# Optimization experiments

Hardware: AMD Instinct MI355X
Metric: run time of the kernel (lower is better)

Reference implementation:

```python
import jax, jax.numpy as jnp
import numpy as np

N_NODES = 100000
N_EDGES = 1600000
D_IN = 64
D_OUT = 64
N_AGGR = 2   # mean, std
N_SCAL = 3   # identity, amplification, attenuation
EPS = 1e-7


def setup_inputs() -> dict:
    key = jax.random.key(0)
    ks = jax.random.split(key, 6)
    x = jax.random.normal(ks[0], (N_NODES, D_IN), dtype=jnp.float32)
    edge_row = jax.random.randint(ks[1], (N_EDGES,), 0, N_NODES)  # dst nodes
    edge_col = jax.random.randint(ks[2], (N_EDGES,), 0, N_NODES)  # src nodes
    # glorot init for linear weights, stored as [out, in] like torch.nn.Linear
    g = np.sqrt(6.0 / (D_IN + D_OUT))
    pre_w = jax.random.uniform(ks[3], (N_AGGR, N_SCAL, D_OUT, D_IN),
                               minval=-g, maxval=g, dtype=jnp.float32)
    lin_w = jax.random.uniform(ks[4], (D_OUT, D_IN), minval=-g, maxval=g,
                               dtype=jnp.float32)
    bias = jnp.zeros((D_OUT,), dtype=jnp.float32)
    # avg_deg['log'] = mean over nodes of log(deg+1); use expected value ~log(17)
    avg_deg_log = jnp.asarray(np.log(17.0), dtype=jnp.float32)
    return {"x": x, "edge_row": edge_row, "edge_col": edge_col,
            "pre_w": pre_w, "lin_w": lin_w, "bias": bias,
            "avg_deg_log": avg_deg_log}


def reference(x, edge_row, edge_col, pre_w, lin_w, bias, avg_deg_log):
    n = x.shape[0]
    # deg = adj_t.storage.rowcount(): number of edges per destination node
    deg = jax.ops.segment_sum(jnp.ones_like(edge_row, dtype=x.dtype),
                              edge_row, num_segments=n)[:, None]  # [N,1]
    # Two SpMM passes: adj_t @ x and adj_t @ x**2 (sum over source neighbors)
    xj = x[edge_col]                                             # [E,D]
    s1 = jax.ops.segment_sum(xj, edge_row, num_segments=n)       # [N,D]
    s2 = jax.ops.segment_sum(xj * xj, edge_row, num_segments=n)  # [N,D]
    mean = s1
    std = jnp.sqrt(jax.nn.relu(s2 - s1 * s1) + EPS)
    agg = jnp.stack([mean, std])                                 # [2,N,D]
    # 6 per-head projections: heads ordered as product(aggregators, scalers)
    proj = jnp.einsum('and,asod->asno', agg, pre_w)              # [2,3,N,O]
    logd = jnp.log(deg + 1.0)                                    # [N,1]
    factors = jnp.stack([
        jnp.ones_like(logd),            # identity
        logd / avg_deg_log,             # amplification
        avg_deg_log / (logd + EPS),     # attenuation
    ])                                                           # [3,N,1]
    out = (proj * factors[None]).sum(axis=(0, 1))                # sum over heads
    out = out + x @ lin_w.T + bias
    return out
```

## Files before the change

kernel.cpp:

```cpp
#include <hip/hip_runtime.h>
#include <cmath>

constexpr int KTOT = 448;
constexpr int KSTEPS = 14;
constexpr int ZROW = 456;
constexpr int NBMAX = 256;
constexpr int BCAP = 12288;

typedef __attribute__((ext_vector_type(8))) short bf16x8;
typedef __attribute__((ext_vector_type(4))) float f32x4;

static __device__ inline ushort bfq(float f) {
  unsigned u = __builtin_bit_cast(unsigned, f);
  return (ushort)((u + 0x7FFFu + ((u >> 16) & 1u)) >> 16);
}
static __device__ inline float b2f(ushort h) {
  return __builtin_bit_cast(float, (unsigned)h << 16);
}
static __device__ inline unsigned pk2(float a, float b) {
  return (unsigned)bfq(a) | ((unsigned)bfq(b) << 16);
}

__global__ void __launch_bounds__(256)
kA_prep(const float* __restrict__ x, ushort* __restrict__ xh,
        const float* __restrict__ pre_w, const float* __restrict__ lin_w,
        float* __restrict__ Wt, ushort* __restrict__ Bfrag,
        int* __restrict__ bcur, int total) {
  int t = threadIdx.x;
  if (blockIdx.x == 0) bcur[t] = t * BCAP;

  int base = blockIdx.x * 2048 + t * 8;
  if (base + 7 < total) {
    const float4* xp = (const float4*)(x + base);
    float4 v0 = xp[0], v1 = xp[1];
    uint4 o;
    o.x = pk2(v0.x, v0.y);
    o.y = pk2(v0.z, v0.w);
    o.z = pk2(v1.x, v1.y);
    o.w = pk2(v1.z, v1.w);
    *(uint4*)(xh + base) = o;
  }

  int idx = blockIdx.x * 256 + t;
  if (idx < KTOT * 64) {
    int k = idx >> 6, o = idx & 63;
    int slot = k >> 6, d = k & 63;
    Wt[idx] = (slot < 6) ? pre_w[slot * 4096 + o * 64 + d] : lin_w[o * 64 + d];
    int j = idx & 7, lane = (idx >> 3) & 63, ot = (idx >> 9) & 3, ks = idx >> 11;
    int kk = ks * 32 + (lane >> 4) * 8 + j;
    int oo = ot * 16 + (lane & 15);
    int s2 = kk >> 6, d2 = kk & 63;
    float v = (s2 < 6) ? pre_w[s2 * 4096 + oo * 64 + d2] : lin_w[oo * 64 + d2];
    Bfrag[idx] = bfq(v);
  }
}

#define BTILE 8192
__global__ void __launch_bounds__(256)
kD_binpass(const int* __restrict__ erow, const int* __restrict__ ecol,
           int* __restrict__ bcur, unsigned* __restrict__ pairs, int ne) {
  __shared__ int h[NBMAX], gb[NBMAX], h2[NBMAX];
  int t = threadIdx.x;
  h[t] = 0; h2[t] = 0;
  __syncthreads();
  int base = blockIdx.x * BTILE;
  int lim = ne - base; if (lim > BTILE) lim = BTILE;
  for (int k = t; k < lim; k += 256)
    atomicAdd(&h[erow[base + k] >> 9], 1);
  __syncthreads();
  if (h[t] > 0) gb[t] = atomicAdd(&bcur[t], h[t]);
  __syncthreads();
  for (int k = t; k < lim; k += 256) {
    int dst = erow[base + k];
    int src = ecol[base + k];
    int b = dst >> 9;
    int r = atomicAdd(&h2[b], 1);
    pairs[gb[b] + r] = ((unsigned)(dst & 511) << 17) | (unsigned)src;
  }
}

__global__ void __launch_bounds__(512)
kE_within(const unsigned* __restrict__ pairs, const int* __restrict__ bcur,
          int2* __restrict__ rr, int* __restrict__ esrc, int nn) {
  __shared__ int lcnt[512], ts[512];
  int b = blockIdx.x;
  int t = threadIdx.x;
  int nstart = b << 9;
  int s = b * BCAP;
  int m = bcur[b] - s;
  lcnt[t] = 0;
  __syncthreads();
  for (int i = t; i < m; i += 512)
    atomicAdd(&lcnt[pairs[s + i] >> 17], 1);
  __syncthreads();
  int v = lcnt[t];
  ts[t] = v;
  __syncthreads();
  for (int off = 1; off < 512; off <<= 1) {
    int u = (t >= off) ? ts[t - off] : 0;
    __syncthreads();
    ts[t] += u;
    __syncthreads();
  }
  int incl = ts[t];
  int n = nstart + t;
  if (n < nn) rr[n] = make_int2(s + incl - v, s + incl);
  lcnt[t] = s + incl - v;
  __syncthreads();
  for (int i = t; i < m; i += 512) {
    unsigned w = pairs[s + i];
    int p = atomicAdd(&lcnt[w >> 17], 1);
    esrc[p] = (int)(w & 0x1FFFFu);
  }
}

static __device__ inline void chunk_acc(const ushort* __restrict__ xh, int sv,
                                        int cnt, int lane, float& a1, float& a2) {
  int k = 0;
  for (; k + 15 < cnt; k += 16) {
    float v[16];
#pragma unroll
    for (int u = 0; u < 16; ++u)
      v[u] = b2f(xh[__shfl(sv, k + u) * 64 + lane]);
#pragma unroll
    for (int u = 0; u < 16; ++u) { a1 += v[u]; a2 = fmaf(v[u], v[u], a2); }
  }
  for (; k + 3 < cnt; k += 4) {
    float v[4];
#pragma unroll
    for (int u = 0; u < 4; ++u)
      v[u] = b2f(xh[__shfl(sv, k + u) * 64 + lane]);
#pragma unroll
    for (int u = 0; u < 4; ++u) { a1 += v[u]; a2 = fmaf(v[u], v[u], a2); }
  }
  for (; k < cnt; ++k) {
    float v = b2f(xh[__shfl(sv, k) * 64 + lane]);
    a1 += v; a2 = fmaf(v, v, a2);
  }
}

__global__ void __launch_bounds__(256, 6)
k_agg_dense(const ushort* __restrict__ xh,
            const int2* __restrict__ rr,
            const int* __restrict__ esrc,
            const ushort* __restrict__ Bfrag,
            const float* __restrict__ Wt,
            const float* __restrict__ bias,
            const float* __restrict__ avgp,
            float* __restrict__ out, int nn) {
  __shared__ __align__(16) ushort zs[16 * ZROW];
  const float avg = avgp[0];
  const int wave = threadIdx.x >> 6, lane = threadIdx.x & 63;
  const int n0 = blockIdx.x * 16;
  const int nw = n0 + wave * 4;

  int2 rv = (lane < 4) ? rr[nw + lane] : make_int2(0, 0);
  int s0 = __shfl(rv.x, 0), t0 = __shfl(rv.y, 0);
  int s1 = __shfl(rv.x, 1), t1 = __shfl(rv.y, 1);
  int s2 = __shfl(rv.x, 2), t2 = __shfl(rv.y, 2);
  int s3 = __shfl(rv.x, 3), t3 = __shfl(rv.y, 3);
  int sv0 = (s0 + lane < t0) ? esrc[s0 + lane] : 0;
  int sv1 = (s1 + lane < t1) ? esrc[s1 + lane] : 0;
  int sv2 = (s2 + lane < t2) ? esrc[s2 + lane] : 0;
  int sv3 = (s3 + lane < t3) ? esrc[s3 + lane] : 0;

  int zmask = 0;

#define DO_NODE(J, SJ, EJ, SVJ)                                              \
  {                                                                          \
    int n = nw + J;                                                          \
    float a1 = 0.f, a2 = 0.f;                                                \
    int nb = EJ - SJ; if (nb > 64) nb = 64;                                  \
    chunk_acc(xh, SVJ, nb, lane, a1, a2);                                    \
    for (int base = SJ + 64; base < EJ; base += 64) {                        \
      int c = EJ - base; if (c > 64) c = 64;                                 \
      int sv = (base + lane < EJ) ? esrc[base + lane] : 0;                   \
      chunk_acc(xh, sv, c, lane, a1, a2);                                    \
    }                                                                        \
    float m = a1;                                                            \
    float sd = sqrtf(fmaxf(a2 - m * m, 0.f) + 1e-7f);                        \
    int deg = EJ - SJ;                                                       \
    if (deg == 0) zmask |= (1 << J);                                         \
    float logd = logf((float)deg + 1.f);                                     \
    float f2 = logd / avg;                                                   \
    float f3 = avg / (logd + 1e-7f);                                         \
    float xv = b2f(xh[n * 64 + lane]);    \
    ushort* zr = zs + (wave * 4 + J) * ZROW;                                 \
    zr[lane]       = bfq(m);                                                 \
    zr[64 + lane]  = bfq(m * f2);                                            \
    zr[128 + lane] = bfq(m * f3);                                            \
    zr[192 + lane] = bfq(sd);                                                \
    zr[256 + lane] = bfq(sd * f2);                                           \
    zr[320 + lane] = bfq(sd * f3);                                           \
    zr[384 + lane] = bfq(xv);                                                \
  }
  DO_NODE(0, s0, t0, sv0)
  DO_NODE(1, s1, t1, sv1)
  DO_NODE(2, s2, t2, sv2)
  DO_NODE(3, s3, t3, sv3)
#undef DO_NODE

  __syncthreads();

  const int r = lane & 15, kg = lane >> 4;
  const ushort* za = zs + r * ZROW + kg * 8;
  const ushort* bp = Bfrag + (wave * 64 + lane) * 8;
  f32x4 acc = {0.f, 0.f, 0.f, 0.f};
#pragma unroll
  for (int ks = 0; ks < KSTEPS; ++ks) {
    bf16x8 a = *(const bf16x8*)(za + ks * 32);
    bf16x8 b = *(const bf16x8*)(bp + ks * 2048);
    acc = __builtin_amdgcn_mfma_f32_16x16x32_bf16(a, b, acc, 0, 0, 0);
  }
  float bc = bias[wave * 16 + r];
#pragma unroll
  for (int i = 0; i < 4; ++i) {
    int n = n0 + kg * 4 + i;
    if (n < nn) out[n * 64 + wave * 16 + r] = acc[i] + bc;
  }

  if (__syncthreads_or(zmask)) {
#pragma unroll
    for (int J = 0; J < 4; ++J) {
      int n = nw + J;
      if ((zmask >> J) & 1 && n < nn) {
        float sd0 = sqrtf(1e-7f);
        float f3z = avg / 1e-7f;
        float accx = bias[lane];
        for (int d = 0; d < 64; ++d) {
          float xd = b2f(xh[n * 64 + d]);
          accx += sd0 * Wt[(192 + d) * 64 + lane]
                + sd0 * f3z * Wt[(320 + d) * 64 + lane]
                + xd * Wt[(384 + d) * 64 + lane];
        }
        out[n * 64 + lane] = accx;
      }
    }
  }
}

extern "C" void kernel_launch(void* const* d_in, const int* in_sizes, int n_in,
                              void* d_out, int out_size, void* d_ws, size_t ws_size,
                              hipStream_t stream) {
  const float* x     = (const float*)d_in[0];
  const int*   erow  = (const int*)d_in[1];
  const int*   ecol  = (const int*)d_in[2];
  const float* pre_w = (const float*)d_in[3];
  const float* lin_w = (const float*)d_in[4];
  const float* bias  = (const float*)d_in[5];
  const float* avgp  = (const float*)d_in[6];
  float* out = (float*)d_out;

  int nn = in_sizes[0] / 64;
  int ne = in_sizes[1];
  int total = nn * 64;
  int nbk = (nn + 511) / 512;

  char* w = (char*)d_ws;
  auto align = [](size_t v) { return (v + 255) & ~(size_t)255; };
  size_t off = 0;
  ushort* xh     = (ushort*)(w + off); off = align(off + (size_t)total * 2);
  int* esrc      = (int*)(w + off); off = align(off + (size_t)NBMAX * BCAP * 4);
  unsigned* prs  = (unsigned*)(w + off); off = align(off + (size_t)NBMAX * BCAP * 4);
  int2* rr       = (int2*)(w + off); off = align(off + (size_t)nn * 8);
  int* bcur      = (int*)(w + off); off = align(off + NBMAX * 4);
  float* Wt      = (float*)(w + off); off = align(off + (size_t)KTOT * 64 * 4);
  ushort* Bfr    = (ushort*)(w + off); off = align(off + (size_t)KSTEPS * 4 * 64 * 8 * 2);
  (void)ws_size;

  int gA = (total + 2047) / 2048;
  kA_prep<<<gA, 256, 0, stream>>>(x, xh, pre_w, lin_w, Wt, Bfr, bcur, total);
  kD_binpass<<<(ne + BTILE - 1) / BTILE, 256, 0, stream>>>(erow, ecol, bcur, prs, ne);
  kE_within<<<nbk, 512, 0, stream>>>(prs, bcur, rr, esrc, nn);
  k_agg_dense<<<(nn + 15) / 16, 256, 0, stream>>>(xh, rr, esrc, Bfr, Wt, bias,
                                                  avgp, out, nn);
}
```

Before: 188.0 us.

## Raise block counts in edge binning and split per-bucket CSR build into halves

The binning pass now uses smaller edge tiles with 512 threads per block, which launches many more blocks. The per-bucket counting-sort kernel now runs two blocks per 512-node bucket, each handling 256 destination nodes and writing into its own half of the bucket's output region. The aim is to fill more of the GPU's compute units during the CSR construction stages. The cost is that each half-block scans the whole bucket's pair list, doubling those reads, and more blocks contend on the global bucket-cursor atomics.

```diff
diff --git a/kernel.cpp b/kernel.cpp
--- a/kernel.cpp
+++ b/kernel.cpp
@@ -55,22 +55,22 @@
   }
 }
 
-#define BTILE 8192
-__global__ void __launch_bounds__(256)
+#define BTILE 2048
+__global__ void __launch_bounds__(512)
 kD_binpass(const int* __restrict__ erow, const int* __restrict__ ecol,
            int* __restrict__ bcur, unsigned* __restrict__ pairs, int ne) {
   __shared__ int h[NBMAX], gb[NBMAX], h2[NBMAX];
   int t = threadIdx.x;
-  h[t] = 0; h2[t] = 0;
+  if (t < NBMAX) { h[t] = 0; h2[t] = 0; }
   __syncthreads();
   int base = blockIdx.x * BTILE;
   int lim = ne - base; if (lim > BTILE) lim = BTILE;
-  for (int k = t; k < lim; k += 256)
+  for (int k = t; k < lim; k += 512)
     atomicAdd(&h[erow[base + k] >> 9], 1);
   __syncthreads();
-  if (h[t] > 0) gb[t] = atomicAdd(&bcur[t], h[t]);
-  __syncthreads();
-  for (int k = t; k < lim; k += 256) {
+  if (t < NBMAX && h[t] > 0) gb[t] = atomicAdd(&bcur[t], h[t]);
+  __syncthreads();
+  for (int k = t; k < lim; k += 512) {
     int dst = erow[base + k];
     int src = ecol[base + k];
     int b = dst >> 9;
@@ -82,35 +82,45 @@
 __global__ void __launch_bounds__(512)
 kE_within(const unsigned* __restrict__ pairs, const int* __restrict__ bcur,
           int2* __restrict__ rr, int* __restrict__ esrc, int nn) {
-  __shared__ int lcnt[512], ts[512];
-  int b = blockIdx.x;
+  __shared__ int lcnt[256], ts[256];
+  int blk = blockIdx.x;
+  int b = blk >> 1, half = blk & 1;
   int t = threadIdx.x;
-  int nstart = b << 9;
+  int nstart = (b << 9) + half * 256;
   int s = b * BCAP;
   int m = bcur[b] - s;
-  lcnt[t] = 0;
-  __syncthreads();
-  for (int i = t; i < m; i += 512)
-    atomicAdd(&lcnt[pairs[s + i] >> 17], 1);
-  __syncthreads();
-  int v = lcnt[t];
-  ts[t] = v;
-  __syncthreads();
-  for (int off = 1; off < 512; off <<= 1) {
-    int u = (t >= off) ? ts[t - off] : 0;
+  int ebase = s + half * (BCAP / 2);
+  int lo = half << 8, hi = lo + 256;
+  if (t < 256) lcnt[t] = 0;
+  __syncthreads();
+  for (int i = t; i < m; i += 512) {
+    int dl = (int)(pairs[s + i] >> 17);
+    if (dl >= lo && dl < hi) atomicAdd(&lcnt[dl - lo], 1);
+  }
+  __syncthreads();
+  int v = 0;
+  if (t < 256) { v = lcnt[t]; ts[t] = v; }
+  __syncthreads();
+  for (int off = 1; off < 256; off <<= 1) {
+    int u = (t >= off && t < 256) ? ts[t - off] : 0;
     __syncthreads();
-    ts[t] += u;
+    if (t < 256) ts[t] += u;
     __syncthreads();
   }
-  int incl = ts[t];
-  int n = nstart + t;
-  if (n < nn) rr[n] = make_int2(s + incl - v, s + incl);
-  lcnt[t] = s + incl - v;
+  if (t < 256) {
+    int incl = ts[t];
+    int n = nstart + t;
+    if (n < nn) rr[n] = make_int2(ebase + incl - v, ebase + incl);
+    lcnt[t] = ebase + incl - v;
+  }
   __syncthreads();
   for (int i = t; i < m; i += 512) {
     unsigned w = pairs[s + i];
-    int p = atomicAdd(&lcnt[w >> 17], 1);
-    esrc[p] = (int)(w & 0x1FFFFu);
+    int dl = (int)(w >> 17);
+    if (dl >= lo && dl < hi) {
+      int p = atomicAdd(&lcnt[dl - lo], 1);
+      esrc[p] = (int)(w & 0x1FFFFu);
+    }
   }
 }
 
@@ -270,8 +280,8 @@
 
   int gA = (total + 2047) / 2048;
   kA_prep<<<gA, 256, 0, stream>>>(x, xh, pre_w, lin_w, Wt, Bfr, bcur, total);
-  kD_binpass<<<(ne + BTILE - 1) / BTILE, 256, 0, stream>>>(erow, ecol, bcur, prs, ne);
-  kE_within<<<nbk, 512, 0, stream>>>(prs, bcur, rr, esrc, nn);
+  kD_binpass<<<(ne + BTILE - 1) / BTILE, 512, 0, stream>>>(erow, ecol, bcur, prs, ne);
+  kE_within<<<nbk * 2, 512, 0, stream>>>(prs, bcur, rr, esrc, nn);
   k_agg_dense<<<(nn + 15) / 16, 256, 0, stream>>>(xh, rr, esrc, Bfr, Wt, bias,
                                                   avgp, out, nn);
 }
```

New measurement: 192.4 us. 2.4% more time.
